# Performance work log

Measured on AMD Instinct MI355X. Metric: run time of the kernel, lower is better.

Reference implementation:

```python
import jax, jax.numpy as jnp
import numpy as np

D_MODEL = 512
DEPTH = 2
D_STATE = 16
D_CONV = 4
EXPAND = 2
D_INNER = EXPAND * D_MODEL
DT_RANK = (D_MODEL + 15) // 16  # ceil(d_model/16) = 32
B_SZ = 8
SEQ = 2048


def setup_inputs() -> dict:
    key = jax.random.key(0)
    ks = jax.random.split(key, 8)
    s = 0.02
    A0 = jnp.log(jnp.broadcast_to(jnp.arange(1, D_STATE + 1, dtype=jnp.float32),
                                  (DEPTH, D_INNER, D_STATE)))
    return {
        "x": jax.random.normal(ks[0], (B_SZ, SEQ, D_MODEL), jnp.float32),
        "ln_w": jnp.ones((DEPTH, D_MODEL), jnp.float32),
        "ln_b": jnp.zeros((DEPTH, D_MODEL), jnp.float32),
        "in_proj_w": jax.random.normal(ks[1], (DEPTH, 2 * D_INNER, D_MODEL), jnp.float32) * s,
        "conv_w": jax.random.normal(ks[2], (DEPTH, D_INNER, 1, D_CONV), jnp.float32) * s,
        "conv_b": jnp.zeros((DEPTH, D_INNER), jnp.float32),
        "x_proj_w": jax.random.normal(ks[3], (DEPTH, DT_RANK + 2 * D_STATE, D_INNER), jnp.float32) * s,
        "dt_proj_w": jax.random.normal(ks[4], (DEPTH, D_INNER, DT_RANK), jnp.float32) * s,
        "dt_proj_b": jax.random.uniform(ks[5], (DEPTH, D_INNER), jnp.float32, -4.0, -2.0),
        "A_log": A0,
        "D_param": jnp.ones((DEPTH, D_INNER), jnp.float32),
        "out_proj_w": jax.random.normal(ks[6], (DEPTH, D_MODEL, D_INNER), jnp.float32) * s,
    }


def _layer_norm(x, w, b):
    mu = x.mean(-1, keepdims=True)
    var = ((x - mu) ** 2).mean(-1, keepdims=True)
    return (x - mu) * jax.lax.rsqrt(var + 1e-5) * w + b


def _mamba_block(x, in_w, cw, cb, xp_w, dtw, dtb, A_log, Dp, ow):
    B = x.shape[0]
    # input projection -> x branch and gate z
    xz = jnp.einsum('bld,ed->ble', x, in_w)          # [B,L,2*d_inner]
    xi, z = jnp.split(xz, 2, axis=-1)
    # depthwise causal conv1d over time
    xc = jnp.transpose(xi, (0, 2, 1))                 # [B,d_inner,L]
    xc = jax.lax.conv_general_dilated(
        xc, cw, (1,), [(D_CONV - 1, 0)],
        dimension_numbers=('NCH', 'OIH', 'NCH'),
        feature_group_count=D_INNER)
    xc = xc + cb[None, :, None]
    xi = jax.nn.silu(jnp.transpose(xc, (0, 2, 1)))    # [B,L,d_inner]
    # input-dependent dt, B, C
    dbc = jnp.einsum('ble,fe->blf', xi, xp_w)         # [B,L,dt_rank+2*d_state]
    dt = dbc[..., :DT_RANK]
    Bm = dbc[..., DT_RANK:DT_RANK + D_STATE]
    Cm = dbc[..., DT_RANK + D_STATE:]
    delta = jax.nn.softplus(jnp.einsum('blr,er->ble', dt, dtw) + dtb)  # [B,L,d_inner]
    A = -jnp.exp(A_log)                               # [d_inner,d_state]

    def step(h, ins):
        d_t, B_t, C_t, u_t = ins                      # [B,E],[B,N],[B,N],[B,E]
        dA = jnp.exp(d_t[..., None] * A)              # [B,E,N]
        h = dA * h + (d_t * u_t)[..., None] * B_t[:, None, :]
        y = jnp.einsum('ben,bn->be', h, C_t)
        return h, y

    h0 = jnp.zeros((B, D_INNER, D_STATE), x.dtype)
    ins = (jnp.transpose(delta, (1, 0, 2)),
           jnp.transpose(Bm, (1, 0, 2)),
           jnp.transpose(Cm, (1, 0, 2)),
           jnp.transpose(xi, (1, 0, 2)))
    _, ys = jax.lax.scan(step, h0, ins)               # ys: [L,B,d_inner]
    y = jnp.transpose(ys, (1, 0, 2)) + xi * Dp        # skip term D*u
    y = y * jax.nn.silu(z)                            # gate
    return jnp.einsum('ble,de->bld', y, ow)           # out projection


def reference(x, ln_w, ln_b, in_proj_w, conv_w, conv_b, x_proj_w,
              dt_proj_w, dt_proj_b, A_log, D_param, out_proj_w):
    for i in range(DEPTH):
        x = x + _mamba_block(_layer_norm(x, ln_w[i], ln_b[i]),
                             in_proj_w[i], conv_w[i], conv_b[i], x_proj_w[i],
                             dt_proj_w[i], dt_proj_b[i], A_log[i], D_param[i],
                             out_proj_w[i])
    return x
```

## Files before the change

kernel.cpp:

```cpp
#include <hip/hip_runtime.h>
#include <hip/hip_bf16.h>
#include <math.h>

#define B_SZ   8
#define SEQ    2048
#define DMODEL 512
#define DEPTH  2
#define DSTATE 16
#define DCONV  4
#define DINNER 1024
#define DTRANK 32
#define ROWS   (B_SZ * SEQ)
#define DBCW   (DTRANK + 2 * DSTATE)

typedef unsigned short u16;
typedef float f32x4 __attribute__((ext_vector_type(4)));
typedef short bf16x8 __attribute__((ext_vector_type(8)));

__device__ __forceinline__ float silu_f(float v) {
    return v * __builtin_amdgcn_rcpf(1.f + __expf(-v));
}
__device__ __forceinline__ float softplus_f(float s) {
    return (s > 20.f) ? s : __logf(1.f + __expf(s));
}
__device__ __forceinline__ u16 f2b(float v) {
    __hip_bfloat16 h = __float2bfloat16(v);
    return *(u16*)&h;
}
__device__ __forceinline__ float b2f(u16 v) {
    __hip_bfloat16 h;
    *(u16*)&h = v;
    return __bfloat162float(h);
}
__device__ __forceinline__ float sum16(float x) {
    x += __int_as_float(__builtin_amdgcn_update_dpp(0, __float_as_int(x), 0x121, 0xf, 0xf, true));
    x += __int_as_float(__builtin_amdgcn_update_dpp(0, __float_as_int(x), 0x122, 0xf, 0xf, true));
    x += __int_as_float(__builtin_amdgcn_update_dpp(0, __float_as_int(x), 0x124, 0xf, 0xf, true));
    x += __int_as_float(__builtin_amdgcn_update_dpp(0, __float_as_int(x), 0x128, 0xf, 0xf, true));
    return x;
}

__device__ __forceinline__ void load_lds16(const void* g, void* l) {
    __builtin_amdgcn_global_load_lds(
        (const __attribute__((address_space(1))) unsigned int*)g,
        (__attribute__((address_space(3))) unsigned int*)l, 16, 0, 0);
}

#define N_INW  (2 * DINNER * DMODEL)
#define N_OUTW (DMODEL * DINNER)
#define N_XW   (DBCW * DINNER)
__global__ __launch_bounds__(256) void conv_weights(const float* __restrict__ iw,
                                                    const float* __restrict__ ow,
                                                    const float* __restrict__ xw,
                                                    u16* __restrict__ inwbf,
                                                    u16* __restrict__ outwbf,
                                                    u16* __restrict__ xwbf) {
    int i = blockIdx.x * 256 + threadIdx.x;
    if (i < N_INW) inwbf[i] = f2b(iw[i]);
    else if (i < N_INW + N_OUTW) outwbf[i - N_INW] = f2b(ow[i - N_INW]);
    else if (i < N_INW + N_OUTW + N_XW) xwbf[i - N_INW - N_OUTW] = f2b(xw[i - N_INW - N_OUTW]);
}

__global__ __launch_bounds__(256) void ln_kernel(const float* __restrict__ x,
                                                 const float* __restrict__ w,
                                                 const float* __restrict__ b,
                                                 u16* __restrict__ out) {
    int r = blockIdx.x;
    int tid = threadIdx.x;
    const float* xr = x + (size_t)r * DMODEL;
    float2 v = *(const float2*)(xr + tid * 2);
    float s = v.x + v.y;
    float s2 = v.x * v.x + v.y * v.y;
    #pragma unroll
    for (int off = 1; off < 64; off <<= 1) {
        s  += __shfl_xor(s, off);
        s2 += __shfl_xor(s2, off);
    }
    __shared__ float ws[4], ws2[4];
    int wid = tid >> 6, lane = tid & 63;
    if (lane == 0) { ws[wid] = s; ws2[wid] = s2; }
    __syncthreads();
    float ts = ws[0] + ws[1] + ws[2] + ws[3];
    float ts2 = ws2[0] + ws2[1] + ws2[2] + ws2[3];
    float mean = ts * (1.f / DMODEL);
    float var = ts2 * (1.f / DMODEL) - mean * mean;
    float inv = rsqrtf(var + 1e-5f);
    out[(size_t)r * DMODEL + tid * 2]     = f2b((v.x - mean) * inv * w[tid * 2] + b[tid * 2]);
    out[(size_t)r * DMODEL + tid * 2 + 1] = f2b((v.y - mean) * inv * w[tid * 2 + 1] + b[tid * 2 + 1]);
}

__global__ __launch_bounds__(256) void gemm_in(const u16* __restrict__ A,
                                               const u16* __restrict__ W,
                                               u16* __restrict__ xi_re,
                                               u16* __restrict__ sz_re) {
    __shared__ u16 As[128 * 32];
    __shared__ u16 Bs[128 * 32];
    const int K = DMODEL;
    int tid = threadIdx.x;
    int wave = tid >> 6, lane = tid & 63;
    int wm = (wave >> 1) * 64, wn = (wave & 1) * 64;
    int m0 = blockIdx.y * 128, n0 = blockIdx.x * 128;
    int srow = lane >> 2, sseg = lane & 3;
    const u16* Ag = A + (size_t)(m0 + wave * 32 + srow) * K + sseg * 8;
    const u16* Wg = W + (size_t)(n0 + wave * 32 + srow) * K + sseg * 8;
    u16* Asw = As + wave * 32 * 32;
    u16* Bsw = Bs + wave * 32 * 32;

    f32x4 acc[4][4] = {};
    int col = lane & 15, quad = lane >> 4;

    for (int k0 = 0; k0 < K; k0 += 32) {
        __syncthreads();
        load_lds16(Ag + k0, Asw);
        load_lds16(Ag + k0 + (size_t)16 * K, Asw + 16 * 32);
        load_lds16(Wg + k0, Bsw);
        load_lds16(Wg + k0 + (size_t)16 * K, Bsw + 16 * 32);
        __syncthreads();
        bf16x8 af[4], bfr[4];
        #pragma unroll
        for (int i = 0; i < 4; ++i) {
            af[i]  = *(const bf16x8*)(As + (wm + i * 16 + col) * 32 + quad * 8);
            bfr[i] = *(const bf16x8*)(Bs + (wn + i * 16 + col) * 32 + quad * 8);
        }
        #pragma unroll
        for (int i = 0; i < 4; ++i)
            #pragma unroll
            for (int j = 0; j < 4; ++j)
                acc[i][j] = __builtin_amdgcn_mfma_f32_16x16x32_bf16(af[i], bfr[j], acc[i][j], 0, 0, 0);
    }
    bool is_z = (n0 >= DINNER);
    u16* dst = is_z ? sz_re : xi_re;
    int nb = n0 & (DINNER - 1);
    #pragma unroll
    for (int i = 0; i < 4; ++i) {
        int gm_base = m0 + wm + i * 16 + quad * 4;
        #pragma unroll
        for (int j = 0; j < 4; ++j) {
            int gn = nb + wn + j * 16 + col;
            #pragma unroll
            for (int r = 0; r < 4; ++r) {
                float v = acc[i][j][r];
                if (is_z) v = silu_f(v);
                dst[(size_t)(gm_base + r) * DINNER + gn] = f2b(v);
            }
        }
    }
}

__global__ __launch_bounds__(256) void gemm_out(const u16* __restrict__ A,
                                                const u16* __restrict__ W,
                                                const float* __restrict__ res,
                                                float* __restrict__ C) {
    __shared__ u16 As[128 * 32];
    __shared__ u16 Bs[128 * 32];
    const int K = DINNER, N = DMODEL;
    int tid = threadIdx.x;
    int wave = tid >> 6, lane = tid & 63;
    int wm = (wave >> 1) * 64, wn = (wave & 1) * 64;
    int m0 = blockIdx.y * 128, n0 = blockIdx.x * 128;
    int srow = lane >> 2, sseg = lane & 3;
    const u16* Ag = A + (size_t)(m0 + wave * 32 + srow) * K + sseg * 8;
    const u16* Wg = W + (size_t)(n0 + wave * 32 + srow) * K + sseg * 8;
    u16* Asw = As + wave * 32 * 32;
    u16* Bsw = Bs + wave * 32 * 32;

    f32x4 acc[4][4] = {};
    int col = lane & 15, quad = lane >> 4;

    for (int k0 = 0; k0 < K; k0 += 32) {
        __syncthreads();
        load_lds16(Ag + k0, Asw);
        load_lds16(Ag + k0 + (size_t)16 * K, Asw + 16 * 32);
        load_lds16(Wg + k0, Bsw);
        load_lds16(Wg + k0 + (size_t)16 * K, Bsw + 16 * 32);
        __syncthreads();
        bf16x8 af[4], bfr[4];
        #pragma unroll
        for (int i = 0; i < 4; ++i) {
            af[i]  = *(const bf16x8*)(As + (wm + i * 16 + col) * 32 + quad * 8);
            bfr[i] = *(const bf16x8*)(Bs + (wn + i * 16 + col) * 32 + quad * 8);
        }
        #pragma unroll
        for (int i = 0; i < 4; ++i)
            #pragma unroll
            for (int j = 0; j < 4; ++j)
                acc[i][j] = __builtin_amdgcn_mfma_f32_16x16x32_bf16(af[i], bfr[j], acc[i][j], 0, 0, 0);
    }
    #pragma unroll
    for (int i = 0; i < 4; ++i) {
        int gm_base = m0 + wm + i * 16 + quad * 4;
        #pragma unroll
        for (int j = 0; j < 4; ++j) {
            int gn = n0 + wn + j * 16 + col;
            #pragma unroll
            for (int r = 0; r < 4; ++r) {
                size_t off = (size_t)(gm_base + r) * N + gn;
                C[off] = acc[i][j][r] + res[off];
            }
        }
    }
}

__global__ __launch_bounds__(256) void gemm_xp_bf16(const u16* __restrict__ A,
                                                    const u16* __restrict__ W,
                                                    float* __restrict__ C) {
    __shared__ u16 As[128 * 32];
    __shared__ u16 Bs[64 * 32];
    int tid = threadIdx.x;
    int wave = tid >> 6, lane = tid & 63;
    int m0 = blockIdx.x * 128;
    int wm = wave * 32;
    int srow = lane >> 2, sseg = lane & 3;
    const u16* Ag = A + (size_t)(m0 + wm + srow) * DINNER + sseg * 8;
    const u16* Wg = W + (size_t)(wave * 16 + srow) * DINNER + sseg * 8;
    u16* Asw = As + wave * 32 * 32;
    u16* Bsw = Bs + wave * 16 * 32;

    f32x4 acc[2][4] = {};
    int col = lane & 15, quad = lane >> 4;

    for (int k0 = 0; k0 < DINNER; k0 += 32) {
        __syncthreads();
        load_lds16(Ag + k0, Asw);
        load_lds16(Ag + k0 + (size_t)16 * DINNER, Asw + 16 * 32);
        load_lds16(Wg + k0, Bsw);
        __syncthreads();
        bf16x8 af[2], bfr[4];
        #pragma unroll
        for (int i = 0; i < 2; ++i)
            af[i] = *(const bf16x8*)(As + (wm + i * 16 + col) * 32 + quad * 8);
        #pragma unroll
        for (int j = 0; j < 4; ++j)
            bfr[j] = *(const bf16x8*)(Bs + (j * 16 + col) * 32 + quad * 8);
        #pragma unroll
        for (int i = 0; i < 2; ++i)
            #pragma unroll
            for (int j = 0; j < 4; ++j)
                acc[i][j] = __builtin_amdgcn_mfma_f32_16x16x32_bf16(af[i], bfr[j], acc[i][j], 0, 0, 0);
    }
    #pragma unroll
    for (int i = 0; i < 2; ++i) {
        int gm_base = m0 + wm + i * 16 + quad * 4;
        #pragma unroll
        for (int j = 0; j < 4; ++j) {
            int gn = j * 16 + col;
            #pragma unroll
            for (int r = 0; r < 4; ++r)
                C[(size_t)(gm_base + r) * DBCW + gn] = acc[i][j][r];
        }
    }
}

__global__ __launch_bounds__(256) void u_t_kernel(const u16* __restrict__ xi_re,
                                                  const u16* __restrict__ sz_re,
                                                  const float* __restrict__ cw,
                                                  const float* __restrict__ cb,
                                                  u16* __restrict__ ut,
                                                  u16* __restrict__ u_re,
                                                  u16* __restrict__ szt) {
    __shared__ float xt[67][65];
    __shared__ u16 uo[64][70];
    __shared__ u16 szo[64][70];
    int tid = threadIdx.x;
    int t0 = blockIdx.x * 64, e0 = blockIdx.y * 64, b = blockIdx.z;
    int er = tid & 63, rr = tid >> 6;
    for (int it = 0; it < 17; ++it) {
        int row = it * 4 + rr;
        if (row < 67) {
            int t = t0 + row - 3;
            xt[row][er] = (t >= 0) ? b2f(xi_re[((size_t)b * SEQ + t) * DINNER + e0 + er]) : 0.f;
        }
    }
    #pragma unroll
    for (int it = 0; it < 16; ++it) {
        int row = it * 4 + rr;
        szo[er][row] = sz_re[((size_t)b * SEQ + t0 + row) * DINNER + e0 + er];
    }
    __syncthreads();
    {
        int e = tid & 63, tg = tid >> 6;
        float4 w4 = *(const float4*)(cw + (e0 + e) * 4);
        float cbe = cb[e0 + e];
        int tl0 = tg * 16;
        float x3 = xt[tl0][e], x2 = xt[tl0 + 1][e], x1 = xt[tl0 + 2][e];
        #pragma unroll
        for (int i = 0; i < 16; ++i) {
            float x0 = xt[tl0 + i + 3][e];
            float u = silu_f(cbe + w4.x * x3 + w4.y * x2 + w4.z * x1 + w4.w * x0);
            x3 = x2; x2 = x1; x1 = x0;
            u16 ub = f2b(u);
            uo[e][tl0 + i] = ub;
            u_re[((size_t)b * SEQ + t0 + tl0 + i) * DINNER + e0 + e] = ub;
        }
    }
    __syncthreads();
    {
        int tl = tid & 63, eg = tid >> 6;
        #pragma unroll
        for (int i = 0; i < 16; ++i) {
            int ee = eg * 16 + i;
            ut[((size_t)b * DINNER + e0 + ee) * SEQ + t0 + tl] = uo[ee][tl];
            szt[((size_t)b * DINNER + e0 + ee) * SEQ + t0 + tl] = szo[ee][tl];
        }
    }
}

__global__ __launch_bounds__(256) void delta_bct_kernel(const float* __restrict__ dbc,
                                                        const float* __restrict__ dtw,
                                                        const float* __restrict__ dtb,
                                                        u16* __restrict__ dlt,
                                                        u16* __restrict__ Bt,
                                                        u16* __restrict__ Ct) {
    __shared__ float wl[64 * 32];
    __shared__ float bl[64];
    int tid = threadIdx.x;
    int e0 = blockIdx.x * 64, t0 = blockIdx.y * 256, b = blockIdx.z;
    for (int i = tid; i < 64 * 32; i += 256) wl[i] = dtw[(size_t)e0 * DTRANK + i];
    if (tid < 64) bl[tid] = dtb[e0 + tid];
    float dreg[32];
    const float* dp = dbc + (size_t)(b * SEQ + t0 + tid) * DBCW;
    #pragma unroll
    for (int k = 0; k < 32; k += 4) {
        float4 v = *(const float4*)(dp + k);
        dreg[k] = v.x; dreg[k + 1] = v.y; dreg[k + 2] = v.z; dreg[k + 3] = v.w;
    }
    __syncthreads();
    for (int ep = 0; ep < 64; ++ep) {
        float s = bl[ep];
        #pragma unroll
        for (int k = 0; k < 32; ++k) s += dreg[k] * wl[ep * 32 + k];
        dlt[((size_t)b * DINNER + e0 + ep) * SEQ + t0 + tid] = f2b(softplus_f(s));
    }
    if (blockIdx.x == 0) {
        int t = t0 + tid;
        const float* dp2 = dbc + (size_t)(b * SEQ + t) * DBCW + DTRANK;
        #pragma unroll
        for (int nn = 0; nn < DSTATE; ++nn) {
            Bt[((size_t)b * DSTATE + nn) * SEQ + t] = f2b(dp2[nn]);
            Ct[((size_t)b * DSTATE + nn) * SEQ + t] = f2b(dp2[DSTATE + nn]);
        }
    }
}

#define SCHUNK 16

__global__ __launch_bounds__(256, 2) void scan_fused(u16* __restrict__ y_re,
                                                     const u16* __restrict__ ut,
                                                     const u16* __restrict__ dlt,
                                                     const u16* __restrict__ Bt,
                                                     const u16* __restrict__ Ct,
                                                     const u16* __restrict__ szt,
                                                     const float* __restrict__ Alog,
                                                     const float* __restrict__ Dp) {
    int tid = threadIdx.x;
    int pair = tid >> 4, n = tid & 15;
    int blk = blockIdx.x;
    int b = blk >> 6;
    int e = ((blk & 63) << 4) + pair;
    float a2 = -__expf(Alog[e * DSTATE + n]) * 1.44269504f;
    float dpe = Dp[e];
    const u16* urow  = ut  + ((size_t)b * DINNER + e) * SEQ;
    const u16* dlrow = dlt + ((size_t)b * DINNER + e) * SEQ;
    const u16* szrow = szt + ((size_t)b * DINNER + e) * SEQ;
    const u16* Brow  = Bt + ((size_t)b * DSTATE + n) * SEQ;
    const u16* Crow  = Ct + ((size_t)b * DSTATE + n) * SEQ;
    u16* ystore = y_re + ((size_t)b * SEQ + n) * DINNER + e;

    float h = 0.f;
    bf16x8 Au0, Au1, Adl0, Adl1, AB0, AB1, AC0, AC1;
    bf16x8 Bu0, Bu1, Bdl0, Bdl1, BB0, BB1, BC0, BC1;
    float Asz, Bsz;

    auto load = [&](int c, bf16x8& u0, bf16x8& u1, bf16x8& d0, bf16x8& d1,
                    bf16x8& b0, bf16x8& b1, bf16x8& c0, bf16x8& c1, float& sz) {
        u0 = *(const bf16x8*)(urow + c * SCHUNK);
        u1 = *(const bf16x8*)(urow + c * SCHUNK + 8);
        d0 = *(const bf16x8*)(dlrow + c * SCHUNK);
        d1 = *(const bf16x8*)(dlrow + c * SCHUNK + 8);
        b0 = *(const bf16x8*)(Brow + c * SCHUNK);
        b1 = *(const bf16x8*)(Brow + c * SCHUNK + 8);
        c0 = *(const bf16x8*)(Crow + c * SCHUNK);
        c1 = *(const bf16x8*)(Crow + c * SCHUNK + 8);
        sz = b2f(szrow[c * SCHUNK + n]);
    };
    auto proc = [&](int c, bf16x8 u0, bf16x8 u1, bf16x8 d0, bf16x8 d1,
                    bf16x8 b0, bf16x8 b1, bf16x8 c0, bf16x8 c1, float sz) {
        float keep = 0.f;
        #pragma unroll
        for (int j = 0; j < SCHUNK; ++j) {
            float uf = b2f((u16)((j < 8) ? u0[j] : u1[j - 8]));
            float dl = b2f((u16)((j < 8) ? d0[j] : d1[j - 8]));
            float dA = __builtin_amdgcn_exp2f(dl * a2);
            h = dA * h + (dl * uf) * b2f((u16)((j < 8) ? b0[j] : b1[j - 8]));
            float yp = sum16(h * b2f((u16)((j < 8) ? c0[j] : c1[j - 8])));
            float yg = yp + uf * dpe;
            keep = (n == j) ? yg : keep;
        }
        ystore[(size_t)c * SCHUNK * DINNER] = f2b(keep * sz);
    };

    const int nc = SEQ / SCHUNK;
    load(0, Au0, Au1, Adl0, Adl1, AB0, AB1, AC0, AC1, Asz);
    for (int c = 0; c < nc; c += 2) {
        load(c + 1, Bu0, Bu1, Bdl0, Bdl1, BB0, BB1, BC0, BC1, Bsz);
        proc(c, Au0, Au1, Adl0, Adl1, AB0, AB1, AC0, AC1, Asz);
        if (c + 2 < nc) load(c + 2, Au0, Au1, Adl0, Adl1, AB0, AB1, AC0, AC1, Asz);
        proc(c + 1, Bu0, Bu1, Bdl0, Bdl1, BB0, BB1, BC0, BC1, Bsz);
    }
}

extern "C" void kernel_launch(void* const* d_in, const int* in_sizes, int n_in,
                              void* d_out, int out_size, void* d_ws, size_t ws_size,
                              hipStream_t stream) {
    const float* x_in   = (const float*)d_in[0];
    const float* ln_w   = (const float*)d_in[1];
    const float* ln_b   = (const float*)d_in[2];
    const float* inw    = (const float*)d_in[3];
    const float* convw  = (const float*)d_in[4];
    const float* convb  = (const float*)d_in[5];
    const float* xpw    = (const float*)d_in[6];
    const float* dtw    = (const float*)d_in[7];
    const float* dtb    = (const float*)d_in[8];
    const float* Alog   = (const float*)d_in[9];
    const float* Dp     = (const float*)d_in[10];
    const float* outw   = (const float*)d_in[11];
    float* out = (float*)d_out;

    char* p = (char*)d_ws;
    u16* xi_re = (u16*)p;               p += (size_t)ROWS * DINNER * 2;
    u16* sz_re = (u16*)p;               p += (size_t)ROWS * DINNER * 2;
    u16* y_re  = (u16*)p;               p += (size_t)ROWS * DINNER * 2;
    float* dbc = (float*)p;             p += (size_t)ROWS * DBCW * 4;
    u16* dlt   = (u16*)p;               p += (size_t)B_SZ * DINNER * SEQ * 2;
    u16* u_re  = dlt;
    u16* Bt    = (u16*)p;               p += (size_t)B_SZ * DSTATE * SEQ * 2;
    u16* xwbf  = Bt;
    u16* Ct    = (u16*)p;               p += (size_t)B_SZ * DSTATE * SEQ * 2;
    u16* ut    = (u16*)p;               p += (size_t)B_SZ * DINNER * SEQ * 2;
    u16* xnbf  = ut;
    u16* szt   = (u16*)p;               p += (size_t)B_SZ * DINNER * SEQ * 2;
    u16* inwbf = (u16*)p;               p += (size_t)N_INW * 2;
    u16* outwbf = (u16*)p;              p += (size_t)N_OUTW * 2;

    const dim3 blk256(256);
    const int n_conv = N_INW + N_OUTW + N_XW;

    for (int i = 0; i < DEPTH; ++i) {
        const float* x_cur = (i == 0) ? x_in : out;
        const float* lw  = ln_w  + (size_t)i * DMODEL;
        const float* lb  = ln_b  + (size_t)i * DMODEL;
        const float* iw  = inw   + (size_t)i * 2 * DINNER * DMODEL;
        const float* cw  = convw + (size_t)i * DINNER * DCONV;
        const float* cb  = convb + (size_t)i * DINNER;
        const float* xw  = xpw   + (size_t)i * DBCW * DINNER;
        const float* dw  = dtw   + (size_t)i * DINNER * DTRANK;
        const float* db  = dtb   + (size_t)i * DINNER;
        const float* Al  = Alog  + (size_t)i * DINNER * DSTATE;
        const float* Dpp = Dp    + (size_t)i * DINNER;
        const float* ow  = outw  + (size_t)i * DMODEL * DINNER;

        conv_weights<<<(n_conv + 255) / 256, blk256, 0, stream>>>(
            iw, ow, xw, inwbf, outwbf, xwbf);
        ln_kernel<<<ROWS, blk256, 0, stream>>>(x_cur, lw, lb, xnbf);
        gemm_in<<<dim3(2 * DINNER / 128, ROWS / 128), blk256, 0, stream>>>(
            xnbf, inwbf, xi_re, sz_re);
        u_t_kernel<<<dim3(SEQ / 64, DINNER / 64, B_SZ), blk256, 0, stream>>>(
            xi_re, sz_re, cw, cb, ut, u_re, szt);
        gemm_xp_bf16<<<ROWS / 128, blk256, 0, stream>>>(u_re, xwbf, dbc);
        delta_bct_kernel<<<dim3(DINNER / 64, SEQ / 256, B_SZ), blk256, 0, stream>>>(
            dbc, dw, db, dlt, Bt, Ct);
        scan_fused<<<(B_SZ * DINNER) / 16, blk256, 0, stream>>>(
            y_re, ut, dlt, Bt, Ct, szt, Al, Dpp);
        gemm_out<<<dim3(DMODEL / 128, ROWS / 128), blk256, 0, stream>>>(
            y_re, outwbf, x_cur, out);
    }
}
```

Measured before the change: 854.0 us.

## Deepen scan prefetch to four rotating buffers with sched barriers and mask-select

```diff
diff --git a/kernel.cpp b/kernel.cpp
--- a/kernel.cpp
+++ b/kernel.cpp
@@ -344,6 +344,11 @@
 
 #define SCHUNK 16
 
+struct ChunkBuf {
+    bf16x8 u0, u1, d0, d1, b0, b1, c0, c1;
+    u16 uo_r, szo_r;
+};
+
 __global__ __launch_bounds__(256, 2) void scan_fused(u16* __restrict__ y_re,
                                                      const u16* __restrict__ ut,
                                                      const u16* __restrict__ dlt,
@@ -366,46 +371,54 @@
     const u16* Crow  = Ct + ((size_t)b * DSTATE + n) * SEQ;
     u16* ystore = y_re + ((size_t)b * SEQ + n) * DINNER + e;
 
+    float msk[16];
+    #pragma unroll
+    for (int j = 0; j < 16; ++j) msk[j] = (n == j) ? 1.f : 0.f;
+
     float h = 0.f;
-    bf16x8 Au0, Au1, Adl0, Adl1, AB0, AB1, AC0, AC1;
-    bf16x8 Bu0, Bu1, Bdl0, Bdl1, BB0, BB1, BC0, BC1;
-    float Asz, Bsz;
-
-    auto load = [&](int c, bf16x8& u0, bf16x8& u1, bf16x8& d0, bf16x8& d1,
-                    bf16x8& b0, bf16x8& b1, bf16x8& c0, bf16x8& c1, float& sz) {
-        u0 = *(const bf16x8*)(urow + c * SCHUNK);
-        u1 = *(const bf16x8*)(urow + c * SCHUNK + 8);
-        d0 = *(const bf16x8*)(dlrow + c * SCHUNK);
-        d1 = *(const bf16x8*)(dlrow + c * SCHUNK + 8);
-        b0 = *(const bf16x8*)(Brow + c * SCHUNK);
-        b1 = *(const bf16x8*)(Brow + c * SCHUNK + 8);
-        c0 = *(const bf16x8*)(Crow + c * SCHUNK);
-        c1 = *(const bf16x8*)(Crow + c * SCHUNK + 8);
-        sz = b2f(szrow[c * SCHUNK + n]);
+    ChunkBuf bufA, bufB, bufC, bufD;
+
+    auto load = [&](int c, ChunkBuf& R) {
+        R.u0 = *(const bf16x8*)(urow + c * SCHUNK);
+        R.u1 = *(const bf16x8*)(urow + c * SCHUNK + 8);
+        R.d0 = *(const bf16x8*)(dlrow + c * SCHUNK);
+        R.d1 = *(const bf16x8*)(dlrow + c * SCHUNK + 8);
+        R.b0 = *(const bf16x8*)(Brow + c * SCHUNK);
+        R.b1 = *(const bf16x8*)(Brow + c * SCHUNK + 8);
+        R.c0 = *(const bf16x8*)(Crow + c * SCHUNK);
+        R.c1 = *(const bf16x8*)(Crow + c * SCHUNK + 8);
+        R.uo_r  = urow[c * SCHUNK + n];
+        R.szo_r = szrow[c * SCHUNK + n];
     };
-    auto proc = [&](int c, bf16x8 u0, bf16x8 u1, bf16x8 d0, bf16x8 d1,
-                    bf16x8 b0, bf16x8 b1, bf16x8 c0, bf16x8 c1, float sz) {
+    auto proc = [&](int c, const ChunkBuf& R) {
         float keep = 0.f;
         #pragma unroll
         for (int j = 0; j < SCHUNK; ++j) {
-            float uf = b2f((u16)((j < 8) ? u0[j] : u1[j - 8]));
-            float dl = b2f((u16)((j < 8) ? d0[j] : d1[j - 8]));
+            float uf = b2f((u16)((j < 8) ? R.u0[j] : R.u1[j - 8]));
+            float dl = b2f((u16)((j < 8) ? R.d0[j] : R.d1[j - 8]));
             float dA = __builtin_amdgcn_exp2f(dl * a2);
-            h = dA * h + (dl * uf) * b2f((u16)((j < 8) ? b0[j] : b1[j - 8]));
-            float yp = sum16(h * b2f((u16)((j < 8) ? c0[j] : c1[j - 8])));
-            float yg = yp + uf * dpe;
-            keep = (n == j) ? yg : keep;
-        }
-        ystore[(size_t)c * SCHUNK * DINNER] = f2b(keep * sz);
+            h = dA * h + (dl * uf) * b2f((u16)((j < 8) ? R.b0[j] : R.b1[j - 8]));
+            float yp = sum16(h * b2f((u16)((j < 8) ? R.c0[j] : R.c1[j - 8])));
+            keep += yp * msk[j];
+        }
+        ystore[(size_t)c * SCHUNK * DINNER] =
+            f2b((keep + b2f(R.uo_r) * dpe) * b2f(R.szo_r));
     };
 
     const int nc = SEQ / SCHUNK;
-    load(0, Au0, Au1, Adl0, Adl1, AB0, AB1, AC0, AC1, Asz);
-    for (int c = 0; c < nc; c += 2) {
-        load(c + 1, Bu0, Bu1, Bdl0, Bdl1, BB0, BB1, BC0, BC1, Bsz);
-        proc(c, Au0, Au1, Adl0, Adl1, AB0, AB1, AC0, AC1, Asz);
-        if (c + 2 < nc) load(c + 2, Au0, Au1, Adl0, Adl1, AB0, AB1, AC0, AC1, Asz);
-        proc(c + 1, Bu0, Bu1, Bdl0, Bdl1, BB0, BB1, BC0, BC1, Bsz);
+    load(0, bufA);
+    load(1, bufB);
+    load(2, bufC);
+    __builtin_amdgcn_sched_barrier(0);
+    for (int c = 0; c < nc; c += 4) {
+        int c3 = c + 3, c4 = c + 4, c5 = c + 5, c6 = c + 6;
+        c4 = (c4 < nc) ? c4 : nc - 1;
+        c5 = (c5 < nc) ? c5 : nc - 1;
+        c6 = (c6 < nc) ? c6 : nc - 1;
+        load(c3, bufD);  __builtin_amdgcn_sched_barrier(0);  proc(c,     bufA);
+        load(c4, bufA);  __builtin_amdgcn_sched_barrier(0);  proc(c + 1, bufB);
+        load(c5, bufB);  __builtin_amdgcn_sched_barrier(0);  proc(c + 2, bufC);
+        load(c6, bufC);  __builtin_amdgcn_sched_barrier(0);  proc(c + 3, bufD);
     }
 }
 
```

New measurement: 860.9 us. Within noise of the previous version (+0.8%).
